# Kernel tuning notes

Measured on AMD Instinct MI355X. Metric: run time of the kernel, lower is better.

The kernel has to match this reference:

```python
import jax, jax.numpy as jnp
import numpy as np

EMBED = 8   # forced: combine_heads Linear(embed_dim, embed_dim) applied to 8-wire measurement
FFN = 32
B, S = 128, 8192
EPS = 1e-5


def _layernorm(x, g, b):
    m = x.mean(-1, keepdims=True)
    v = ((x - m) ** 2).mean(-1, keepdims=True)
    return (x - m) * jax.lax.rsqrt(v + EPS) * g + b


def setup_inputs() -> dict:
    key = jax.random.key(0)
    ks = jax.random.split(key, 8)

    def lin(k, fi, fo):
        return jax.random.normal(k, (fi, fo), jnp.float32) / np.sqrt(fi).astype(np.float32)

    return dict(
        x=jax.random.normal(ks[0], (B, S, EMBED), jnp.float32),
        Wq=lin(ks[1], EMBED, EMBED), bq=jnp.zeros((EMBED,), jnp.float32),
        theta_attn=jax.random.uniform(ks[2], (EMBED,), jnp.float32, -np.pi, np.pi),
        Wc=lin(ks[3], EMBED, EMBED), bc=jnp.zeros((EMBED,), jnp.float32),
        g1=jnp.ones((EMBED,), jnp.float32), beta1=jnp.zeros((EMBED,), jnp.float32),
        theta_ffn=jax.random.uniform(ks[4], (EMBED,), jnp.float32, -np.pi, np.pi),
        W1=lin(ks[5], EMBED, FFN), b1=jnp.zeros((FFN,), jnp.float32),
        W2=lin(ks[6], FFN, EMBED), b2=jnp.zeros((EMBED,), jnp.float32),
        g2=jnp.ones((EMBED,), jnp.float32), beta2=jnp.zeros((EMBED,), jnp.float32),
    )


def reference(x, Wq, bq, theta_attn, Wc, bc, g1, beta1,
              theta_ffn, W1, b1, W2, b2, g2, beta2):
    # --- MultiHeadAttentionQuantum (eval mode, dropout = identity) ---
    # q_linear; the 8-wire encoder consumes all 8 features of q per token.
    q = x @ Wq + bq                           # [B, S, 8]
    # Circuit per token: RX(q_i) then trainable RX(theta_i) on wire i -> RX(q_i+theta_i),
    # then CNOT ring (0->1,...,6->7, 7->0), then <Z_i>.
    # All-RX product state => basis probs p_i(1)=sin^2(a_i/2); CNOTs permute basis
    # states (prefix-XOR of bits), so analytically:
    #   <Z_k> = prod_{j=0..k} cos(a_j)  for k>=1;   <Z_0> = prod_{j=1..7} cos(a_j)
    ca = jnp.cos(q + theta_attn)              # [B, S, 8]
    z_rest = jnp.cumprod(ca, axis=-1)[..., 1:]
    z0 = jnp.prod(ca[..., 1:], axis=-1, keepdims=True)
    z = jnp.concatenate([z0, z_rest], axis=-1)
    attn_out = z @ Wc + bc                    # combine_heads

    x1 = _layernorm(x + attn_out, g1, beta1)

    # --- FeedForwardQuantum: RX(x_i) then RY(theta_i), no entanglers ->
    #     <Z_i> = cos(theta_i) * cos(x_i)  (product state, per-wire closed form)
    zf = jnp.cos(theta_ffn) * jnp.cos(x1)     # [B, S, 8]
    h = jax.nn.relu(zf @ W1 + b1)             # linear1 -> relu
    ffn_out = h @ W2 + b2                     # linear2

    return _layernorm(x1 + ffn_out, g2, beta2)
```

## Files before the change

kernel.cpp:

```cpp
#include <hip/hip_runtime.h>


#define NTOK   (128 * 8192)
#define NTHREADS 256
#define NBLOCKS  (NTOK / NTHREADS)
#define LN_EPS 1e-5f
#define INV2PI 0.15915494309189535f

typedef __fp16 half2_t __attribute__((ext_vector_type(2)));
typedef __fp16 half8_t __attribute__((ext_vector_type(8)));
typedef float  float4_t __attribute__((ext_vector_type(4)));

union PK  { unsigned u; half2_t h; };
union U4H { uint4 u; half8_t h; half2_t h2[4]; };

__device__ __forceinline__ float fast_cos_rev(float xrev) {
    return __builtin_amdgcn_cosf(xrev);
}
__device__ __forceinline__ float fast_cos(float x) {
    return __builtin_amdgcn_cosf(x * INV2PI);
}
__device__ __forceinline__ float fast_rsqrt(float x) {
    return __builtin_amdgcn_rsqf(x);
}
__device__ __forceinline__ unsigned packh2(float a, float b) {
    PK c; c.h = __builtin_amdgcn_cvt_pkrtz(a, b); return c.u;
}
__device__ __forceinline__ float dot2(half2_t a, unsigned bw, float c) {
    PK b; b.u = bw;
    return __builtin_amdgcn_fdot2(a, b.h, c, false);
}

__global__ void pack_weights(const float* __restrict__ Wq,
                             const float* __restrict__ W1,
                             const float* __restrict__ W2,
                             const float* __restrict__ Wc,
                             const float* __restrict__ bq,
                             const float* __restrict__ tha,
                             unsigned* __restrict__ ws)
{
    int idx = threadIdx.x;
    if (idx < 32) {
        int k = idx >> 2, p = idx & 3;
        ws[idx] = packh2(Wq[(2 * p) * 8 + k] * INV2PI, Wq[(2 * p + 1) * 8 + k] * INV2PI);
    } else if (idx < 64) {
        int i2 = idx - 32;
        int kp = i2 >> 3, j = i2 & 7;
        ws[idx] = packh2(Wc[(2 * kp) * 8 + j], Wc[(2 * kp + 1) * 8 + j]);
    } else if (idx < 72) {
        int k = idx - 64;
        ws[idx] = __float_as_uint((bq[k] + tha[k]) * INV2PI);
    } else if (idx >= 128 && idx < 320) {
        int t  = (idx - 128) & 63;
        int tb = (idx - 128) >> 6;
        int n0 = t & 15, q = t >> 4;
        uint4 w = make_uint4(0u, 0u, 0u, 0u);
        unsigned r[4] = {0u, 0u, 0u, 0u};
        if (tb == 0) {
            if (q == 0)
                for (int p = 0; p < 4; ++p)
                    r[p] = packh2(W1[(2 * p) * 32 + n0], W1[(2 * p + 1) * 32 + n0]);
        } else if (tb == 1) {
            if (q == 0)
                for (int p = 0; p < 4; ++p)
                    r[p] = packh2(W1[(2 * p) * 32 + n0 + 16], W1[(2 * p + 1) * 32 + n0 + 16]);
        } else {
            if (n0 < 8)
                for (int p = 0; p < 4; ++p)
                    r[p] = packh2(W2[(8 * q + 2 * p) * 8 + n0], W2[(8 * q + 2 * p + 1) * 8 + n0]);
        }
        w.x = r[0]; w.y = r[1]; w.z = r[2]; w.w = r[3];
        reinterpret_cast<uint4*>(ws)[32 + tb * 64 + t] = w;
    }
}

__global__ __launch_bounds__(NTHREADS, 4)
void qtb_kernel(const float* __restrict__ x,
                const float* __restrict__ bc,
                const float* __restrict__ g1,  const float* __restrict__ be1,
                const float* __restrict__ thf,
                const float* __restrict__ b1,
                const float* __restrict__ b2,
                const float* __restrict__ g2,  const float* __restrict__ be2,
                const unsigned* __restrict__ wp,
                float* __restrict__ out)
{
    const int tid  = threadIdx.x;
    const int wave = tid >> 6;
    const int lane = tid & 63;
    const int col  = lane & 15;
    const int quad = lane >> 4;
    const int g    = blockIdx.x * NTHREADS + tid;
    const float* qb = reinterpret_cast<const float*>(wp + 64);

    __shared__ uint4 zbuf[4][64];
    __shared__ float hbuf[4][16 * 34];
    __shared__ float fbuf[4][64 * 9];

    const uint4* fr = reinterpret_cast<const uint4*>(wp);
    U4H B1a, B1b, B2;
    B1a.u = fr[32 + lane];
    B1b.u = fr[96 + lane];
    B2.u  = fr[160 + lane];
    const float b1a_s = b1[col];
    const float b1b_s = b1[col + 16];
    const float b2_s  = (col < 8) ? b2[col & 7] : 0.f;

    float xv[8];
    half2_t xp[4];
    {
        const float4* p = reinterpret_cast<const float4*>(x) + (size_t)g * 2;
        float4 a = p[0];
        float4 b = p[1];
        xv[0] = a.x; xv[1] = a.y; xv[2] = a.z; xv[3] = a.w;
        xv[4] = b.x; xv[5] = b.y; xv[6] = b.z; xv[7] = b.w;
        xp[0] = __builtin_amdgcn_cvt_pkrtz(a.x, a.y);
        xp[1] = __builtin_amdgcn_cvt_pkrtz(a.z, a.w);
        xp[2] = __builtin_amdgcn_cvt_pkrtz(b.x, b.y);
        xp[3] = __builtin_amdgcn_cvt_pkrtz(b.z, b.w);
    }

    float ca[8];
#pragma unroll
    for (int k = 0; k < 8; ++k) {
        float q = qb[k];
#pragma unroll
        for (int p = 0; p < 4; ++p) q = dot2(xp[p], wp[k * 4 + p], q);
        ca[k] = fast_cos_rev(q);
    }
    float attn[8];
#pragma unroll
    for (int j = 0; j < 8; ++j) attn[j] = bc[j];
    {
        float z[8];
        float cp  = ca[0];
        float cp1 = 1.0f;
#pragma unroll
        for (int k = 1; k < 8; ++k) {
            cp  *= ca[k];
            cp1 *= ca[k];
            z[k] = cp;
        }
        z[0] = cp1;
        half2_t zp[4];
#pragma unroll
        for (int p = 0; p < 4; ++p)
            zp[p] = __builtin_amdgcn_cvt_pkrtz(z[2 * p], z[2 * p + 1]);
#pragma unroll
        for (int p = 0; p < 4; ++p)
#pragma unroll
            for (int j = 0; j < 8; ++j)
                attn[j] = dot2(zp[p], wp[32 + p * 8 + j], attn[j]);
    }

    {
        float y[8];
        float s = 0.f;
#pragma unroll
        for (int j = 0; j < 8; ++j) { y[j] = xv[j] + attn[j]; s += y[j]; }
        float m = s * 0.125f;
        float v = 0.f;
#pragma unroll
        for (int j = 0; j < 8; ++j) { float d = y[j] - m; v += d * d; }
        float r = fast_rsqrt(v * 0.125f + LN_EPS);
        float zf[8];
#pragma unroll
        for (int j = 0; j < 8; ++j) {
            float x1 = (y[j] - m) * r * g1[j] + be1[j];
            xv[j] = x1;
            zf[j] = fast_cos(thf[j]) * fast_cos(x1);
        }
        U4H zpk;
#pragma unroll
        for (int p = 0; p < 4; ++p)
            zpk.h2[p] = __builtin_amdgcn_cvt_pkrtz(zf[2 * p], zf[2 * p + 1]);
        zbuf[wave][lane] = zpk.u;
    }

#pragma unroll
    for (int grp = 0; grp < 4; ++grp) {
        U4H A1; A1.u = zbuf[wave][grp * 16 + col];
        float4_t c1a = {b1a_s, b1a_s, b1a_s, b1a_s};
        float4_t c1b = {b1b_s, b1b_s, b1b_s, b1b_s};
        float4_t h0 = __builtin_amdgcn_mfma_f32_16x16x32_f16(A1.h, B1a.h, c1a, 0, 0, 0);
        float4_t h1 = __builtin_amdgcn_mfma_f32_16x16x32_f16(A1.h, B1b.h, c1b, 0, 0, 0);
#pragma unroll
        for (int r = 0; r < 4; ++r) {
            hbuf[wave][(4 * quad + r) * 34 + col]      = fmaxf(h0[r], 0.f);
            hbuf[wave][(4 * quad + r) * 34 + col + 16] = fmaxf(h1[r], 0.f);
        }
        U4H A2;
#pragma unroll
        for (int p = 0; p < 4; ++p) {
            float ha = hbuf[wave][col * 34 + 8 * quad + 2 * p];
            float hb = hbuf[wave][col * 34 + 8 * quad + 2 * p + 1];
            A2.h2[p] = __builtin_amdgcn_cvt_pkrtz(ha, hb);
        }
        float4_t c2 = {b2_s, b2_s, b2_s, b2_s};
        float4_t f = __builtin_amdgcn_mfma_f32_16x16x32_f16(A2.h, B2.h, c2, 0, 0, 0);
        if (col < 8) {
#pragma unroll
            for (int r = 0; r < 4; ++r)
                fbuf[wave][(grp * 16 + 4 * quad + r) * 9 + col] = f[r];
        }
    }

    {
        float y[8];
        float s = 0.f;
#pragma unroll
        for (int j = 0; j < 8; ++j) {
            y[j] = xv[j] + fbuf[wave][lane * 9 + j];
            s += y[j];
        }
        float m = s * 0.125f;
        float v = 0.f;
#pragma unroll
        for (int j = 0; j < 8; ++j) { float d = y[j] - m; v += d * d; }
        float r = fast_rsqrt(v * 0.125f + LN_EPS);
        float o[8];
#pragma unroll
        for (int j = 0; j < 8; ++j) o[j] = (y[j] - m) * r * g2[j] + be2[j];
        float4* q = reinterpret_cast<float4*>(out) + (size_t)g * 2;
        q[0] = make_float4(o[0], o[1], o[2], o[3]);
        q[1] = make_float4(o[4], o[5], o[6], o[7]);
    }
}

extern "C" void kernel_launch(void* const* d_in, const int* in_sizes, int n_in,
                              void* d_out, int out_size, void* d_ws, size_t ws_size,
                              hipStream_t stream) {
    (void)in_sizes; (void)n_in; (void)ws_size; (void)out_size;
    unsigned* wp = (unsigned*)d_ws;
    pack_weights<<<1, 320, 0, stream>>>(
        (const float*)d_in[1],
        (const float*)d_in[9],
        (const float*)d_in[11],
        (const float*)d_in[4],
        (const float*)d_in[2],
        (const float*)d_in[3],
        wp);
    qtb_kernel<<<NBLOCKS, NTHREADS, 0, stream>>>(
        (const float*)d_in[0],
        (const float*)d_in[5],
        (const float*)d_in[6],
        (const float*)d_in[7],
        (const float*)d_in[8],
        (const float*)d_in[10],
        (const float*)d_in[12],
        (const float*)d_in[13],
        (const float*)d_in[14],
        wp,
        (float*)d_out);
}
```

Baseline: 114.9 us.

## Pack ReLU hidden as fp16 pairs in LDS, precompute cos(theta_ffn), raise occupancy

The ReLU hidden activations are now stored to shared memory as packed fp16 pairs (h0,h1) instead of fp32. They are read back with two 128-bit loads and byte-permuted into the A operand of the second MFMA, which replaces eight scalar LDS reads and four conversions. cos(theta_ffn) is precomputed once in the weight-pack kernel. The x load is hoisted to the top of the kernel, and launch bounds ask for 8 blocks per CU, which raises occupancy but may force register spilling.

Measured after the change: 113.4 us. No clear change (-1.3%).

```diff
diff --git a/kernel.cpp b/kernel.cpp
--- a/kernel.cpp
+++ b/kernel.cpp
@@ -37,6 +37,7 @@
                              const float* __restrict__ Wc,
                              const float* __restrict__ bq,
                              const float* __restrict__ tha,
+                             const float* __restrict__ thf,
                              unsigned* __restrict__ ws)
 {
     int idx = threadIdx.x;
@@ -50,6 +51,9 @@
     } else if (idx < 72) {
         int k = idx - 64;
         ws[idx] = __float_as_uint((bq[k] + tha[k]) * INV2PI);
+    } else if (idx < 80) {
+        int j = idx - 72;
+        ws[idx] = __float_as_uint(__builtin_amdgcn_cosf(thf[j] * INV2PI));
     } else if (idx >= 128 && idx < 320) {
         int t  = (idx - 128) & 63;
         int tb = (idx - 128) >> 6;
@@ -74,11 +78,10 @@
     }
 }
 
-__global__ __launch_bounds__(NTHREADS, 4)
+__global__ __launch_bounds__(NTHREADS, 8)
 void qtb_kernel(const float* __restrict__ x,
                 const float* __restrict__ bc,
                 const float* __restrict__ g1,  const float* __restrict__ be1,
-                const float* __restrict__ thf,
                 const float* __restrict__ b1,
                 const float* __restrict__ b2,
                 const float* __restrict__ g2,  const float* __restrict__ be2,
@@ -91,11 +94,17 @@
     const int col  = lane & 15;
     const int quad = lane >> 4;
     const int g    = blockIdx.x * NTHREADS + tid;
+
+    const float4* px = reinterpret_cast<const float4*>(x) + (size_t)g * 2;
+    float4 xa = px[0];
+    float4 xb = px[1];
+
     const float* qb = reinterpret_cast<const float*>(wp + 64);
-
-    __shared__ uint4 zbuf[4][64];
-    __shared__ float hbuf[4][16 * 34];
-    __shared__ float fbuf[4][64 * 9];
+    const float* cf = reinterpret_cast<const float*>(wp + 72);
+
+    __shared__ uint4    zbuf[4][64];
+    __shared__ unsigned hbuf[4][16 * 20];
+    __shared__ float    fbuf[4][64 * 9];
 
     const uint4* fr = reinterpret_cast<const uint4*>(wp);
     U4H B1a, B1b, B2;
@@ -108,17 +117,12 @@
 
     float xv[8];
     half2_t xp[4];
-    {
-        const float4* p = reinterpret_cast<const float4*>(x) + (size_t)g * 2;
-        float4 a = p[0];
-        float4 b = p[1];
-        xv[0] = a.x; xv[1] = a.y; xv[2] = a.z; xv[3] = a.w;
-        xv[4] = b.x; xv[5] = b.y; xv[6] = b.z; xv[7] = b.w;
-        xp[0] = __builtin_amdgcn_cvt_pkrtz(a.x, a.y);
-        xp[1] = __builtin_amdgcn_cvt_pkrtz(a.z, a.w);
-        xp[2] = __builtin_amdgcn_cvt_pkrtz(b.x, b.y);
-        xp[3] = __builtin_amdgcn_cvt_pkrtz(b.z, b.w);
-    }
+    xv[0] = xa.x; xv[1] = xa.y; xv[2] = xa.z; xv[3] = xa.w;
+    xv[4] = xb.x; xv[5] = xb.y; xv[6] = xb.z; xv[7] = xb.w;
+    xp[0] = __builtin_amdgcn_cvt_pkrtz(xa.x, xa.y);
+    xp[1] = __builtin_amdgcn_cvt_pkrtz(xa.z, xa.w);
+    xp[2] = __builtin_amdgcn_cvt_pkrtz(xb.x, xb.y);
+    xp[3] = __builtin_amdgcn_cvt_pkrtz(xb.z, xb.w);
 
     float ca[8];
 #pragma unroll
@@ -168,7 +172,7 @@
         for (int j = 0; j < 8; ++j) {
             float x1 = (y[j] - m) * r * g1[j] + be1[j];
             xv[j] = x1;
-            zf[j] = fast_cos(thf[j]) * fast_cos(x1);
+            zf[j] = cf[j] * fast_cos(x1);
         }
         U4H zpk;
 #pragma unroll
@@ -177,6 +181,7 @@
         zbuf[wave][lane] = zpk.u;
     }
 
+    const unsigned psel = (quad < 2) ? 0x05040100u : 0x07060302u;
 #pragma unroll
     for (int grp = 0; grp < 4; ++grp) {
         U4H A1; A1.u = zbuf[wave][grp * 16 + col];
@@ -185,17 +190,17 @@
         float4_t h0 = __builtin_amdgcn_mfma_f32_16x16x32_f16(A1.h, B1a.h, c1a, 0, 0, 0);
         float4_t h1 = __builtin_amdgcn_mfma_f32_16x16x32_f16(A1.h, B1b.h, c1b, 0, 0, 0);
 #pragma unroll
-        for (int r = 0; r < 4; ++r) {
-            hbuf[wave][(4 * quad + r) * 34 + col]      = fmaxf(h0[r], 0.f);
-            hbuf[wave][(4 * quad + r) * 34 + col + 16] = fmaxf(h1[r], 0.f);
-        }
+        for (int r = 0; r < 4; ++r)
+            hbuf[wave][(4 * quad + r) * 20 + col] =
+                packh2(fmaxf(h0[r], 0.f), fmaxf(h1[r], 0.f));
+        int hb = col * 20 + (quad & 1) * 8;
+        uint4 w0 = *reinterpret_cast<const uint4*>(&hbuf[wave][hb]);
+        uint4 w1 = *reinterpret_cast<const uint4*>(&hbuf[wave][hb + 4]);
         U4H A2;
-#pragma unroll
-        for (int p = 0; p < 4; ++p) {
-            float ha = hbuf[wave][col * 34 + 8 * quad + 2 * p];
-            float hb = hbuf[wave][col * 34 + 8 * quad + 2 * p + 1];
-            A2.h2[p] = __builtin_amdgcn_cvt_pkrtz(ha, hb);
-        }
+        A2.u.x = __builtin_amdgcn_perm(w0.y, w0.x, psel);
+        A2.u.y = __builtin_amdgcn_perm(w0.w, w0.z, psel);
+        A2.u.z = __builtin_amdgcn_perm(w1.y, w1.x, psel);
+        A2.u.w = __builtin_amdgcn_perm(w1.w, w1.z, psel);
         float4_t c2 = {b2_s, b2_s, b2_s, b2_s};
         float4_t f = __builtin_amdgcn_mfma_f32_16x16x32_f16(A2.h, B2.h, c2, 0, 0, 0);
         if (col < 8) {
@@ -239,13 +244,13 @@
         (const float*)d_in[4],
         (const float*)d_in[2],
         (const float*)d_in[3],
+        (const float*)d_in[8],
         wp);
     qtb_kernel<<<NBLOCKS, NTHREADS, 0, stream>>>(
         (const float*)d_in[0],
         (const float*)d_in[5],
         (const float*)d_in[6],
         (const float*)d_in[7],
-        (const float*)d_in[8],
         (const float*)d_in[10],
         (const float*)d_in[12],
         (const float*)d_in[13],
```
